# Optimization experiments

Measured on AMD Instinct MI355X. Metric: run time of the kernel, lower is better.

## Reference

```python
import jax, jax.numpy as jnp
import numpy as np

B, IN_DIM, EMBED_DIM = 8192, 2048, 256
H1, H2 = 1024, 512
CODEBOOK_SIZE, N_LAYERS = 1024, 3
TEMP, COMMIT_W = 1.25, 0.25


def _l2norm(x, eps=1e-12):
    # F.normalize: x / max(||x||, eps)
    n = jnp.linalg.norm(x, axis=-1, keepdims=True)
    return x / jnp.maximum(n, eps)


def _layernorm(x, g, b, eps=1e-5):
    mu = x.mean(-1, keepdims=True)
    var = x.var(-1, keepdims=True)  # biased, matches torch LayerNorm
    return (x - mu) / jnp.sqrt(var + eps) * g + b


def _mlp(x, w1, g1, b1, w2, g2, b2, w3, normalize):
    h = _layernorm(jax.nn.silu(x @ w1), g1, b1)
    h = _layernorm(jax.nn.silu(h @ w2), g2, b2)
    h = h @ w3
    return _l2norm(h) if normalize else h


def _quantize(res, codebook, key):
    # squared euclidean distances [B, K], scaled by temperature
    dist = ((res ** 2).sum(1, keepdims=True)
            + (codebook ** 2).sum(1)[None, :]
            - 2.0 * res @ codebook.T) / TEMP
    # torch.multinomial(softmax(-dist)) == categorical with logits -dist
    ids = jax.random.categorical(key, -dist, axis=1)
    emb = codebook[ids]  # [B, D] gather
    sg = jax.lax.stop_gradient
    u = res / (jnp.linalg.norm(res, axis=-1, keepdims=True) + 1e-8)
    q = emb / (jnp.linalg.norm(emb, axis=-1, keepdims=True) + 1e-8)
    w = sg(_l2norm(u + q, eps=1e-6))
    # rotation trick: e - 2(e.w)w + 2(e.u)q  (w, u, q detached)
    emb_out = (res
               - 2.0 * (res * w).sum(-1, keepdims=True) * w
               + 2.0 * (res * sg(u)).sum(-1, keepdims=True) * sg(q))
    # QuantizeLoss (sum-reduced MSE both directions)
    loss = ((sg(res) - emb) ** 2).sum() + COMMIT_W * ((res - sg(emb)) ** 2).sum()
    return emb_out, ids, loss


def setup_inputs() -> dict:
    key = jax.random.key(0)
    ks = jax.random.split(key, 8)
    def lin(k, fan_in, fan_out):
        return (jax.random.normal(k, (fan_in, fan_out), jnp.float32)
                / np.sqrt(fan_in).astype(np.float32))
    return {
        "x": jax.random.normal(ks[0], (B, IN_DIM), jnp.float32),
        "enc_w1": lin(ks[1], IN_DIM, H1),
        "enc_g1": jnp.ones((H1,), jnp.float32),
        "enc_b1": jnp.zeros((H1,), jnp.float32),
        "enc_w2": lin(ks[2], H1, H2),
        "enc_g2": jnp.ones((H2,), jnp.float32),
        "enc_b2": jnp.zeros((H2,), jnp.float32),
        "enc_w3": lin(ks[3], H2, EMBED_DIM),
        "dec_w1": lin(ks[4], EMBED_DIM, H2),
        "dec_g1": jnp.ones((H2,), jnp.float32),
        "dec_b1": jnp.zeros((H2,), jnp.float32),
        "dec_w2": lin(ks[5], H2, H1),
        "dec_g2": jnp.ones((H1,), jnp.float32),
        "dec_b2": jnp.zeros((H1,), jnp.float32),
        "dec_w3": lin(ks[6], H1, IN_DIM),
        # nn.init.uniform_ -> U[0,1)
        "codebooks": jax.random.uniform(ks[7], (N_LAYERS, CODEBOOK_SIZE, EMBED_DIM), jnp.float32),
    }


def reference(x, enc_w1, enc_g1, enc_b1, enc_w2, enc_g2, enc_b2, enc_w3,
              dec_w1, dec_g1, dec_b1, dec_w2, dec_g2, dec_b2, dec_w3,
              codebooks):
    res = _mlp(x, enc_w1, enc_g1, enc_b1, enc_w2, enc_g2, enc_b2, enc_w3,
               normalize=False)
    keys = jax.random.split(jax.random.key(42), N_LAYERS)
    quant_loss = jnp.float32(0.0)
    embs, sem = [], []
    for i in range(N_LAYERS):  # small fixed residual depth
        e, ids, l = _quantize(res, codebooks[i], keys[i])
        quant_loss = quant_loss + l
        res = res - e
        embs.append(e)
        sem.append(ids)
    embs_arr = jnp.stack(embs, axis=-1)   # [B, D, L]
    sem_ids = jnp.stack(sem, axis=-1)     # [B, L]
    x_hat = _mlp(embs_arr.sum(-1), dec_w1, dec_g1, dec_b1, dec_w2, dec_g2,
                 dec_b2, dec_w3, normalize=True)
    recon = ((x_hat - x) ** 2).sum(-1)    # per-sample [B]
    loss = (recon + quant_loss).mean()
    embs_norm = jnp.linalg.norm(embs_arr, axis=1)  # [B, L]
    eq = (sem_ids[:, None, :] == sem_ids[None, :, :]).all(-1)  # [B, B]
    p_unique = (~jnp.triu(eq, k=1)).all(1).sum() / sem_ids.shape[0]
    return loss, recon.mean(), quant_loss, embs_norm, p_unique
```

## Files before the change

kernel.cpp:

```cpp
#include <hip/hip_runtime.h>
#include <hip/hip_bf16.h>
#include <stdint.h>
#include <math.h>

#define NB    8192
#define INDIM 2048
#define EMB   256
#define H1N   1024
#define H2N   512
#define KCB   1024
#define NLAYER 3
#define HASHN 16384

typedef _Float16 f16x8 __attribute__((ext_vector_type(8)));
typedef _Float16 f16x4 __attribute__((ext_vector_type(4)));
typedef _Float16 f16x2 __attribute__((ext_vector_type(2)));
typedef float    f32x4 __attribute__((ext_vector_type(4)));

#define LO_SCALE 1024.0f
#define LO_INV   (1.0f / 1024.0f)

#define GLD16(g, p) __builtin_amdgcn_global_load_lds( \
    (const __attribute__((address_space(1))) void*)(g), \
    (__attribute__((address_space(3))) void*)(p), 16, 0, 0)

__host__ __device__ inline void tf2x32(uint32_t k0, uint32_t k1, uint32_t x0, uint32_t x1,
                                       uint32_t& o0, uint32_t& o1)
{
  const uint32_t ks2 = 0x1BD11BDAu ^ k0 ^ k1;
  uint32_t a = x0 + k0, b = x1 + k1;
#define TF_RND(r) { a += b; b = (b << (r)) | (b >> (32 - (r))); b ^= a; }
  TF_RND(13) TF_RND(15) TF_RND(26) TF_RND(6)
  a += k1; b += ks2 + 1u;
  TF_RND(17) TF_RND(29) TF_RND(16) TF_RND(24)
  a += ks2; b += k0 + 2u;
  TF_RND(13) TF_RND(15) TF_RND(26) TF_RND(6)
  a += k0; b += k1 + 3u;
  TF_RND(17) TF_RND(29) TF_RND(16) TF_RND(24)
  a += k1; b += ks2 + 4u;
  TF_RND(13) TF_RND(15) TF_RND(26) TF_RND(6)
  a += ks2; b += k0 + 5u;
#undef TF_RND
  o0 = a; o1 = b;
}

__device__ inline float blk_reduce_sum(float v, float* sbuf)
{
  const int t = threadIdx.x;
  sbuf[t] = v; __syncthreads();
  for (int s = 128; s > 0; s >>= 1) {
    if (t < s) sbuf[t] += sbuf[t + s];
    __syncthreads();
  }
  float r = sbuf[0];
  __syncthreads();
  return r;
}

template<int NS, int OUTMODE, int BM>
__global__ __launch_bounds__(BM == 256 ? 512 : 256) void mgemm(
    const _Float16* __restrict__ A0, const _Float16* __restrict__ A1,
    const _Float16* __restrict__ B0, const _Float16* __restrict__ B1,
    void* __restrict__ Cp, _Float16* __restrict__ Cs0, _Float16* __restrict__ Cs1,
    float* __restrict__ pval, int* __restrict__ pidx, const float* __restrict__ cn2l,
    uint32_t gk0, uint32_t gk1,
    int M, int N, int K)
{
  constexpr int WAVES = (BM == 256) ? 8 : 4;
  constexpr int RPR = WAVES * 16;
  constexpr int AR = BM / RPR;
  constexpr int BR = 128 / RPR;
  constexpr int JN = (BM == 64) ? 2 : 4;
  constexpr int ASPL = BM * 64;
  constexpr int ABYTES = NS * ASPL;
  constexpr int BBYTES = NS * 8192;
  constexpr int BUF = ABYTES + BBYTES;
  __shared__ __align__(16) char sm[2 * BUF];

  const int nwg = gridDim.x * gridDim.y;
  const int bid0 = blockIdx.y * gridDim.x + blockIdx.x;
  const int cpx = nwg >> 3;
  const int swz = (bid0 & 7) * cpx + (bid0 >> 3);
  const int bx = swz % gridDim.x, by = swz / gridDim.x;

  const int tid = threadIdx.x;
  const int w = tid >> 6, l = tid & 63;
  const int wm = (BM == 64) ? 0 : (w >> 1);
  const int wn = (BM == 64) ? w : (w & 1);
  constexpr int WCOL = (BM == 64) ? 32 : 64;
  const size_t brow = (size_t)by * BM;
  const size_t bcol = (size_t)bx * 128;

  const int brow16 = w * 16 + (l >> 2);
  const int bcol16 = ((l & 3) ^ ((l >> 3) & 3)) * 8;

  const _Float16* gA0 = A0 + (brow + brow16) * (size_t)K + bcol16;
  const _Float16* gA1 = (NS >= 2) ? (A1 + (brow + brow16) * (size_t)K + bcol16) : nullptr;
  const _Float16* gB0 = B0 + (bcol + brow16) * (size_t)K + bcol16;
  const _Float16* gB1 = (NS >= 2) ? (B1 + (bcol + brow16) * (size_t)K + bcol16) : nullptr;

  auto STAGE = [&](int buf, int kk) {
    char* bA = sm + buf * BUF;
    char* bB = bA + ABYTES;
#pragma unroll
    for (int i = 0; i < AR; i++) {
      GLD16(gA0 + (size_t)(i * RPR) * K + kk, bA + i * (RPR * 64) + w * 1024);
      if constexpr (NS >= 2) GLD16(gA1 + (size_t)(i * RPR) * K + kk, bA + ASPL + i * (RPR * 64) + w * 1024);
    }
#pragma unroll
    for (int i = 0; i < BR; i++) {
      GLD16(gB0 + (size_t)(i * RPR) * K + kk, bB + i * (RPR * 64) + w * 1024);
      if constexpr (NS >= 2) GLD16(gB1 + (size_t)(i * RPR) * K + kk, bB + 8192 + i * (RPR * 64) + w * 1024);
    }
  };

  f32x4 acc0[4][JN], acc1[4][JN];
#pragma unroll
  for (int i = 0; i < 4; i++)
#pragma unroll
    for (int j = 0; j < JN; j++) {
      acc0[i][j] = (f32x4){0.f, 0.f, 0.f, 0.f};
      if constexpr (NS >= 2) acc1[i][j] = (f32x4){0.f, 0.f, 0.f, 0.f};
    }

  const int srow = l & 15;
  const int ksel = l >> 4;
  const int sel2 = (srow >> 1) & 3;
  const int fslot16 = (ksel ^ sel2) * 16;

  STAGE(0, 0);
  __syncthreads();
  int cur = 0;

  for (int k0 = 0; k0 < K; k0 += 32) {
    if (k0 + 32 < K) STAGE(cur ^ 1, k0 + 32);

    const char* smA = sm + cur * BUF;
    const char* smB = smA + ABYTES;

    f16x8 ah[4], al[4];
#pragma unroll
    for (int i = 0; i < 4; i++) {
      const int rb = (wm * 64 + i * 16 + srow) * 64 + fslot16;
      ah[i] = *(const f16x8*)(smA + rb);
      if constexpr (NS >= 2) al[i] = *(const f16x8*)(smA + ASPL + rb);
    }

#pragma unroll
    for (int j = 0; j < JN; j++) {
      const int rb = (wn * WCOL + j * 16 + srow) * 64 + fslot16;
      f16x8 bh = *(const f16x8*)(smB + rb);
      f16x8 bl{};
      if constexpr (NS >= 2) bl = *(const f16x8*)(smB + 8192 + rb);
#pragma unroll
      for (int i = 0; i < 4; i++) {
        acc0[i][j] = __builtin_amdgcn_mfma_f32_16x16x32_f16(ah[i], bh, acc0[i][j], 0, 0, 0);
        if constexpr (NS >= 2) {
          acc1[i][j] = __builtin_amdgcn_mfma_f32_16x16x32_f16(ah[i], bl, acc1[i][j], 0, 0, 0);
          acc1[i][j] = __builtin_amdgcn_mfma_f32_16x16x32_f16(al[i], bh, acc1[i][j], 0, 0, 0);
        }
      }
    }
    __syncthreads();
    cur ^= 1;
  }

  if constexpr (OUTMODE == 3) {
    const int rowb = (int)brow + wm * 64 + (l >> 4) * 4;
    const int colb = (int)bcol + wn * 64 + (l & 15);
#pragma unroll
    for (int i = 0; i < 4; i++)
#pragma unroll
      for (int r = 0; r < 4; r++) {
        const int grow = rowb + i * 16 + r;
        float bestv = -INFINITY; int bestj = 0x7fffffff;
#pragma unroll
        for (int j = 0; j < JN; j++) {
          float v = acc0[i][j][r];
          if constexpr (NS >= 2) v += acc1[i][j][r] * LO_INV;
          const int gcol = colb + j * 16;
          const uint32_t idx = (uint32_t)(grow * KCB + gcol);
          uint32_t o0, o1;
          tf2x32(gk0, gk1, 0u, idx, o0, o1);
          const uint32_t bits = o0 ^ o1;
          float f = __uint_as_float((bits >> 9) | 0x3f800000u) - 1.0f;
          float u = fmaxf(f, 1.17549435e-38f);
          float gmb = -__logf(-__logf(u));
          float val = gmb + (2.0f * v - cn2l[gcol]) / 1.25f;
          if (val > bestv || (val == bestv && gcol < bestj)) { bestv = val; bestj = gcol; }
        }
#pragma unroll
        for (int m = 1; m < 16; m <<= 1) {
          float ov = __shfl_xor(bestv, m);
          int oj = __shfl_xor(bestj, m);
          if (ov > bestv || (ov == bestv && oj < bestj)) { bestv = ov; bestj = oj; }
        }
        if ((l & 15) == 0) {
          const int slot = bx * 2 + wn;
          pval[(size_t)grow * 16 + slot] = bestv;
          pidx[(size_t)grow * 16 + slot] = bestj;
        }
      }
  } else {
    const int crow0 = wm * 64 + (l >> 4) * 4;
    const int ccol0 = wn * WCOL + (l & 15);
#pragma unroll
    for (int i = 0; i < 4; i++)
#pragma unroll
      for (int j = 0; j < JN; j++)
#pragma unroll
        for (int r = 0; r < 4; r++) {
          float v = acc0[i][j][r];
          if constexpr (NS >= 2) v += acc1[i][j][r] * LO_INV;
          const size_t row = brow + crow0 + i * 16 + r;
          const size_t col = bcol + ccol0 + j * 16;
          const size_t o = row * N + col;
          if constexpr (OUTMODE == 0) {
            ((float*)Cp)[o] = v;
          } else if constexpr (OUTMODE == 1) {
            ((_Float16*)Cp)[o] = (_Float16)v;
          } else {
            ((float*)Cp)[o] = v;
            _Float16 h = (_Float16)v;
            Cs0[o] = h;
            Cs1[o] = (_Float16)((v - (float)h) * LO_SCALE);
          }
        }
  }
}

struct PrepArgs {
  const float* w[6];
  _Float16* t0[6];
  _Float16* t1[6];
  int K[6], N[6];
  int off[7];
  const float* x;
  _Float16* xh; _Float16* xl;
  const float* cb;
  _Float16* cbh; _Float16* cbl;
  float* cn2;
  int cvtBlocks;
};

__global__ __launch_bounds__(256) void prep_all(PrepArgs P)
{
  __shared__ float shf[33 * 32];
  const int b = blockIdx.x, t = threadIdx.x;

  if (b < P.off[6]) {
    int j = 0;
    while (b >= P.off[j + 1]) j++;
    const int lb = b - P.off[j];
    const int K = P.K[j], N = P.N[j];
    const int nbx = N / 32;
    const int nb = (lb % nbx) * 32, kb = (lb / nbx) * 32;
    const float* Wsrc = P.w[j];
    _Float16* T0 = P.t0[j];
    _Float16* T1 = P.t1[j];
    const int tx = t & 31, ty = t >> 5;
#pragma unroll
    for (int i = 0; i < 32; i += 8)
      shf[(ty + i) * 33 + tx] = Wsrc[(size_t)(kb + ty + i) * N + nb + tx];
    __syncthreads();
#pragma unroll
    for (int i = 0; i < 32; i += 8) {
      float v = shf[tx * 33 + ty + i];
      size_t o = (size_t)(nb + ty + i) * K + kb + tx;
      _Float16 h = (_Float16)v;
      T0[o] = h;
      if (T1) T1[o] = (_Float16)((v - (float)h) * LO_SCALE);
    }
  } else if (b < P.off[6] + P.cvtBlocks) {
    const int i = ((b - P.off[6]) * 256 + t) * 8;
    float4 va = *(const float4*)(P.x + i);
    float4 vb = *(const float4*)(P.x + i + 4);
    float f[8] = {va.x, va.y, va.z, va.w, vb.x, vb.y, vb.z, vb.w};
    f16x8 hv, lv;
#pragma unroll
    for (int e = 0; e < 8; e++) {
      _Float16 h = (_Float16)f[e];
      hv[e] = h;
      lv[e] = (_Float16)((f[e] - (float)h) * LO_SCALE);
    }
    *(f16x8*)(P.xh + i) = hv;
    *(f16x8*)(P.xl + i) = lv;
  } else {
    const int r = b - P.off[6] - P.cvtBlocks;
    const size_t o = (size_t)r * EMB + t;
    const float v = P.cb[o];
    _Float16 h = (_Float16)v;
    P.cbh[o] = h;
    P.cbl[o] = (_Float16)((v - (float)h) * LO_SCALE);
    float s = blk_reduce_sum(v * v, shf);
    if (t == 0) P.cn2[r] = s;
  }
}

template<int NCOL, int NS>
__global__ __launch_bounds__(256) void silu_ln(const float* __restrict__ in,
                                               const float* __restrict__ g,
                                               const float* __restrict__ bta,
                                               _Float16* __restrict__ o0,
                                               _Float16* __restrict__ o1)
{
  constexpr int PT = NCOL / 256;
  __shared__ float sb[256];
  const int b = blockIdx.x, t = threadIdx.x;
  const float* row = in + (size_t)b * NCOL;
  const int c0 = t * PT;
  float v[PT];
  if constexpr (PT == 4) {
    float4 xv = *(const float4*)(row + c0);
    v[0] = xv.x; v[1] = xv.y; v[2] = xv.z; v[3] = xv.w;
  } else {
    float2 xv = *(const float2*)(row + c0);
    v[0] = xv.x; v[1] = xv.y;
  }
  float s = 0.f;
#pragma unroll
  for (int i = 0; i < PT; i++) {
    float sv = v[i] / (1.f + expf(-v[i]));
    v[i] = sv; s += sv;
  }
  s = blk_reduce_sum(s, sb);
  const float mu = s / (float)NCOL;
  float q = 0.f;
#pragma unroll
  for (int i = 0; i < PT; i++) { float d = v[i] - mu; q += d * d; }
  q = blk_reduce_sum(q, sb);
  const float inv = 1.f / sqrtf(q / (float)NCOL + 1e-5f);

  float gv[PT], bv[PT];
  if constexpr (PT == 4) {
    float4 g4 = *(const float4*)(g + c0);
    float4 b4 = *(const float4*)(bta + c0);
    gv[0]=g4.x; gv[1]=g4.y; gv[2]=g4.z; gv[3]=g4.w;
    bv[0]=b4.x; bv[1]=b4.y; bv[2]=b4.z; bv[3]=b4.w;
  } else {
    float2 g2 = *(const float2*)(g + c0);
    float2 b2 = *(const float2*)(bta + c0);
    gv[0]=g2.x; gv[1]=g2.y; bv[0]=b2.x; bv[1]=b2.y;
  }
  const size_t ob = (size_t)b * NCOL + c0;
  if constexpr (PT == 4) {
    f16x4 h4, l4;
#pragma unroll
    for (int i = 0; i < 4; i++) {
      float y = (v[i] - mu) * inv * gv[i] + bv[i];
      _Float16 h = (_Float16)y;
      h4[i] = h;
      if constexpr (NS >= 2) l4[i] = (_Float16)((y - (float)h) * LO_SCALE);
    }
    *(f16x4*)(o0 + ob) = h4;
    if constexpr (NS >= 2) *(f16x4*)(o1 + ob) = l4;
  } else {
    f16x2 h2, l2;
#pragma unroll
    for (int i = 0; i < 2; i++) {
      float y = (v[i] - mu) * inv * gv[i] + bv[i];
      _Float16 h = (_Float16)y;
      h2[i] = h;
      if constexpr (NS >= 2) l2[i] = (_Float16)((y - (float)h) * LO_SCALE);
    }
    *(f16x2*)(o0 + ob) = h2;
    if constexpr (NS >= 2) *(f16x2*)(o1 + ob) = l2;
  }
}

__global__ __launch_bounds__(256) void sample_update(
    const float* __restrict__ pval, const int* __restrict__ pidx,
    const float* __restrict__ cbf,
    float* __restrict__ res, float* __restrict__ esum,
    float* __restrict__ qrow, float* __restrict__ outEn,
    _Float16* __restrict__ r0, _Float16* __restrict__ r1,
    _Float16* __restrict__ esumb, int* __restrict__ ids,
    uint32_t* __restrict__ packed, int layer)
{
  __shared__ float sv[256];
  __shared__ int   si[256];
  const int b = blockIdx.x, t = threadIdx.x;

  float best = -INFINITY; int bestj = 0x7fffffff;
  if (t < 16) { best = pval[(size_t)b * 16 + t]; bestj = pidx[(size_t)b * 16 + t]; }
  sv[t] = best; si[t] = bestj; __syncthreads();
  for (int s = 128; s > 0; s >>= 1) {
    if (t < s) {
      float v2 = sv[t + s]; int j2 = si[t + s];
      if (v2 > sv[t] || (v2 == sv[t] && j2 < si[t])) { sv[t] = v2; si[t] = j2; }
    }
    __syncthreads();
  }
  const int id = si[0];
  if (t == 0) {
    ids[b * NLAYER + layer] = id;
    if (layer == NLAYER - 1)
      packed[b] = (uint32_t)ids[b * NLAYER] | ((uint32_t)ids[b * NLAYER + 1] << 10)
                | ((uint32_t)id << 20);
  }
  __syncthreads();

  const size_t idx = (size_t)b * EMB + t;
  const float r = res[idx];
  const float e_ = cbf[(size_t)id * EMB + t];

  const float rn2 = blk_reduce_sum(r * r, sv);
  const float en2 = blk_reduce_sum(e_ * e_, sv);
  const float rn = sqrtf(rn2), en = sqrtf(en2);
  const float u = r / (rn + 1e-8f);
  const float q = e_ / (en + 1e-8f);
  const float sm = u + q;
  const float sn2 = blk_reduce_sum(sm * sm, sv);
  const float w = sm / fmaxf(sqrtf(sn2), 1e-6f);
  const float rw = blk_reduce_sum(r * w, sv);
  const float ru = blk_reduce_sum(r * u, sv);
  const float e = r - 2.f * rw * w + 2.f * ru * q;
  const float eo2 = blk_reduce_sum(e * e, sv);
  const float dq = r - e_;
  const float ql = blk_reduce_sum(dq * dq, sv);

  if (t == 0) {
    outEn[b * NLAYER + layer] = sqrtf(eo2);
    if (layer == 0) qrow[b] = 1.25f * ql; else qrow[b] += 1.25f * ql;
  }
  const float nr = r - e;
  res[idx] = nr;
  if (layer != NLAYER - 1) {
    _Float16 h = (_Float16)nr;
    r0[idx] = h;
    r1[idx] = (_Float16)((nr - (float)h) * LO_SCALE);
  }
  float ns = (layer == 0) ? e : esum[idx] + e;
  esum[idx] = ns;
  if (layer == NLAYER - 1) esumb[idx] = (_Float16)ns;
}

__global__ __launch_bounds__(256) void l2norm_recon(const _Float16* __restrict__ y,
                                                    const float* __restrict__ x,
                                                    float* __restrict__ recon)
{
  __shared__ float sb[256];
  const int b = blockIdx.x, t = threadIdx.x;
  const _Float16* yr = y + (size_t)b * INDIM;
  const float* xr = x + (size_t)b * INDIM;
  f16x8 v = *(const f16x8*)&yr[t * 8];
  float vy[8];
  float ss = 0.f;
#pragma unroll
  for (int i = 0; i < 8; i++) { vy[i] = (float)v[i]; ss += vy[i] * vy[i]; }
  ss = blk_reduce_sum(ss, sb);
  const float inv = 1.f / fmaxf(sqrtf(ss), 1e-12f);
  float4 xa = *(const float4*)&xr[t * 8];
  float4 xb = *(const float4*)&xr[t * 8 + 4];
  float xf[8] = {xa.x, xa.y, xa.z, xa.w, xb.x, xb.y, xb.z, xb.w};
  float acc = 0.f;
#pragma unroll
  for (int i = 0; i < 8; i++) {
    float d = vy[i] * inv - xf[i];
    acc += d * d;
  }
  acc = blk_reduce_sum(acc, sb);
  if (t == 0) recon[b] = acc;
}

__global__ __launch_bounds__(256) void finalize2(const float* __restrict__ recon,
                                                 const float* __restrict__ qrow,
                                                 const uint32_t* __restrict__ packed,
                                                 float* __restrict__ out)
{
  __shared__ uint32_t tab[HASHN];
  __shared__ double sd[256];
  __shared__ int    si[256];
  const int t = threadIdx.x;
  for (int i = t; i < HASHN; i += 256) tab[i] = 0xFFFFFFFFu;
  __syncthreads();

  int my = 0;
  double aR = 0.0, aQ = 0.0;
  for (int i = t; i < NB; i += 256) {
    aR += (double)recon[i];
    aQ += (double)qrow[i];
    const uint32_t v = packed[i];
    uint32_t h = (v * 2654435761u) & (HASHN - 1);
    while (true) {
      uint32_t old = atomicCAS(&tab[h], 0xFFFFFFFFu, v);
      if (old == 0xFFFFFFFFu) { my++; break; }
      if (old == v) break;
      h = (h + 1) & (HASHN - 1);
    }
  }
  sd[t] = aR; si[t] = my; __syncthreads();
  for (int s = 128; s > 0; s >>= 1) {
    if (t < s) { sd[t] += sd[t + s]; si[t] += si[t + s]; }
    __syncthreads();
  }
  const double sumR = sd[0]; const int dcnt = si[0]; __syncthreads();
  sd[t] = aQ; __syncthreads();
  for (int s = 128; s > 0; s >>= 1) { if (t < s) sd[t] += sd[t + s]; __syncthreads(); }
  const double sumQ = sd[0];
  if (t == 0) {
    const float rm = (float)(sumR / (double)NB);
    const float ql = (float)sumQ;
    out[0] = rm + ql;
    out[1] = rm;
    out[2] = ql;
    out[3 + NB * NLAYER] = (float)dcnt / (float)NB;
  }
}

extern "C" void kernel_launch(void* const* d_in, const int* in_sizes, int n_in,
                              void* d_out, int out_size, void* d_ws, size_t ws_size,
                              hipStream_t stream)
{
  const float* x      = (const float*)d_in[0];
  const float* enc_w1 = (const float*)d_in[1];
  const float* enc_g1 = (const float*)d_in[2];
  const float* enc_b1 = (const float*)d_in[3];
  const float* enc_w2 = (const float*)d_in[4];
  const float* enc_g2 = (const float*)d_in[5];
  const float* enc_b2 = (const float*)d_in[6];
  const float* enc_w3 = (const float*)d_in[7];
  const float* dec_w1 = (const float*)d_in[8];
  const float* dec_g1 = (const float*)d_in[9];
  const float* dec_b1 = (const float*)d_in[10];
  const float* dec_w2 = (const float*)d_in[11];
  const float* dec_g2 = (const float*)d_in[12];
  const float* dec_b2 = (const float*)d_in[13];
  const float* dec_w3 = (const float*)d_in[14];
  const float* codebooks = (const float*)d_in[15];
  float* out = (float*)d_out;

  char* W = (char*)d_ws;
  _Float16* xh   = (_Float16*)(W + 0);
  _Float16* h1n0 = (_Float16*)(W + 0);
  _Float16* h1n1 = (_Float16*)(W + 16777216);
  _Float16* h2n0 = (_Float16*)(W + 0);
  _Float16* h2n1 = (_Float16*)(W + 8388608);
  _Float16* res0 = (_Float16*)(W + 16777216);
  _Float16* res1 = (_Float16*)(W + 20971520);
  _Float16* d1n  = (_Float16*)(W + 0);
  _Float16* d2n  = (_Float16*)(W + 25165824);
  _Float16* xl    = (_Float16*)(W + 33554432);
  float*    h2    = (float*)  (W + 33554432);
  float*    d1    = (float*)  (W + 33554432);
  float*    res32 = (float*)  (W + 50331648);
  float*    esum32= (float*)  (W + 58720256);
  float*    h1 = (float*)    (W + 67108864);
  float*    d2 = (float*)    (W + 67108864);
  _Float16* yb = (_Float16*) (W + 67108864);
  _Float16* w1t0 = (_Float16*)(W + 100663296);
  _Float16* w1t1 = (_Float16*)(W + 104857600);
  _Float16* w2t0 = (_Float16*)(W + 109051904);
  _Float16* w2t1 = (_Float16*)(W + 110100480);
  _Float16* w3t0 = (_Float16*)(W + 111149056);
  _Float16* w3t1 = (_Float16*)(W + 111411200);
  _Float16* dw1t = (_Float16*)(W + 111673344);
  _Float16* dw2t = (_Float16*)(W + 111935488);
  _Float16* dw3t = (_Float16*)(W + 112984064);
  _Float16* cbh  = (_Float16*)(W + 117178368);
  _Float16* cbl  = (_Float16*)(W + 118751232);
  _Float16* esumb= (_Float16*)(W + 120324096);
  float* cn2   = (float*)(W + 124518400);
  float* recon = (float*)(W + 124534784);
  float* qrow  = (float*)(W + 124567552);
  int*   ids   = (int*)  (W + 124600320);
  uint32_t* packed = (uint32_t*)(W + 124698624);
  float*    pval   = (float*)   (W + 124850176);
  int*      pidx   = (int*)     (W + 125374464);

  uint32_t key0[NLAYER], key1[NLAYER];
  for (int l = 0; l < NLAYER; l++) tf2x32(0u, 42u, 0u, (uint32_t)l, key0[l], key1[l]);

  dim3 blk(256), blk512(512);
  PrepArgs P;
  P.w[0] = enc_w1; P.t0[0] = w1t0; P.t1[0] = w1t1; P.K[0] = INDIM; P.N[0] = H1N;
  P.w[1] = enc_w2; P.t0[1] = w2t0; P.t1[1] = w2t1; P.K[1] = H1N;   P.N[1] = H2N;
  P.w[2] = enc_w3; P.t0[2] = w3t0; P.t1[2] = w3t1; P.K[2] = H2N;   P.N[2] = EMB;
  P.w[3] = dec_w1; P.t0[3] = dw1t; P.t1[3] = nullptr; P.K[3] = EMB; P.N[3] = H2N;
  P.w[4] = dec_w2; P.t0[4] = dw2t; P.t1[4] = nullptr; P.K[4] = H2N; P.N[4] = H1N;
  P.w[5] = dec_w3; P.t0[5] = dw3t; P.t1[5] = nullptr; P.K[5] = H1N; P.N[5] = INDIM;
  P.off[0] = 0;
  for (int j = 0; j < 6; j++) P.off[j + 1] = P.off[j] + (P.N[j] / 32) * (P.K[j] / 32);
  P.x = x; P.xh = xh; P.xl = xl;
  P.cb = codebooks; P.cbh = cbh; P.cbl = cbl; P.cn2 = cn2;
  P.cvtBlocks = (NB * INDIM) / 2048;
  const int prepGrid = P.off[6] + P.cvtBlocks + NLAYER * KCB;
  prep_all<<<prepGrid, blk, 0, stream>>>(P);

  mgemm<2,0,256><<<dim3(H1N/128, NB/256), blk512, 0, stream>>>(xh, xl, w1t0, w1t1,
      h1, nullptr, nullptr, nullptr, nullptr, nullptr, 0u, 0u, NB, H1N, INDIM);
  silu_ln<H1N,2><<<NB, blk, 0, stream>>>(h1, enc_g1, enc_b1, h1n0, h1n1);
  mgemm<2,0,128><<<dim3(H2N/128, NB/128), blk, 0, stream>>>(h1n0, h1n1, w2t0, w2t1,
      h2, nullptr, nullptr, nullptr, nullptr, nullptr, 0u, 0u, NB, H2N, H1N);
  silu_ln<H2N,2><<<NB, blk, 0, stream>>>(h2, enc_g2, enc_b2, h2n0, h2n1);
  mgemm<2,2,64><<<dim3(EMB/128, NB/64), blk, 0, stream>>>(h2n0, h2n1, w3t0, w3t1,
      res32, res0, res1, nullptr, nullptr, nullptr, 0u, 0u, NB, EMB, H2N);

  for (int l = 0; l < NLAYER; l++) {
    const float* cbfl = codebooks + (size_t)l * KCB * EMB;
    const size_t co = (size_t)l * KCB * EMB;
    mgemm<2,3,256><<<dim3(KCB/128, NB/256), blk512, 0, stream>>>(res0, res1,
        cbh + co, cbl + co, nullptr, nullptr, nullptr,
        pval, pidx, cn2 + l * KCB, key0[l], key1[l], NB, KCB, EMB);
    sample_update<<<NB, blk, 0, stream>>>(pval, pidx, cbfl,
        res32, esum32, qrow, out + 3, res0, res1, esumb, ids, packed, l);
  }

  mgemm<1,0,128><<<dim3(H2N/128, NB/128), blk, 0, stream>>>(esumb, nullptr, dw1t, nullptr,
      d1, nullptr, nullptr, nullptr, nullptr, nullptr, 0u, 0u, NB, H2N, EMB);
  silu_ln<H2N,1><<<NB, blk, 0, stream>>>(d1, dec_g1, dec_b1, d1n, nullptr);
  mgemm<1,0,128><<<dim3(H1N/128, NB/128), blk, 0, stream>>>(d1n, nullptr, dw2t, nullptr,
      d2, nullptr, nullptr, nullptr, nullptr, nullptr, 0u, 0u, NB, H1N, H2N);
  silu_ln<H1N,1><<<NB, blk, 0, stream>>>(d2, dec_g2, dec_b2, d2n, nullptr);
  mgemm<1,1,256><<<dim3(INDIM/128, NB/256), blk512, 0, stream>>>(d2n, nullptr, dw3t, nullptr,
      yb, nullptr, nullptr, nullptr, nullptr, nullptr, 0u, 0u, NB, INDIM, H1N);
  l2norm_recon<<<NB, blk, 0, stream>>>(yb, x, recon);

  finalize2<<<1, blk, 0, stream>>>(recon, qrow, packed, out);
}
```

Baseline: 615.7 us.

## Use packed atomicMax argmax, wave-per-row reductions, and fp16 decoder intermediates

```diff
diff --git a/kernel.cpp b/kernel.cpp
--- a/kernel.cpp
+++ b/kernel.cpp
@@ -57,12 +57,19 @@
   return r;
 }
 
+__device__ inline float wred(float v)
+{
+#pragma unroll
+  for (int m = 32; m > 0; m >>= 1) v += __shfl_xor(v, m);
+  return v;
+}
+
 template<int NS, int OUTMODE, int BM>
 __global__ __launch_bounds__(BM == 256 ? 512 : 256) void mgemm(
     const _Float16* __restrict__ A0, const _Float16* __restrict__ A1,
     const _Float16* __restrict__ B0, const _Float16* __restrict__ B1,
     void* __restrict__ Cp, _Float16* __restrict__ Cs0, _Float16* __restrict__ Cs1,
-    float* __restrict__ pval, int* __restrict__ pidx, const float* __restrict__ cn2l,
+    unsigned long long* __restrict__ amax, const float* __restrict__ cn2l,
     uint32_t gk0, uint32_t gk1,
     int M, int N, int K)
 {
@@ -196,9 +203,11 @@
           if (ov > bestv || (ov == bestv && oj < bestj)) { bestv = ov; bestj = oj; }
         }
         if ((l & 15) == 0) {
-          const int slot = bx * 2 + wn;
-          pval[(size_t)grow * 16 + slot] = bestv;
-          pidx[(size_t)grow * 16 + slot] = bestj;
+          uint32_t mb = __float_as_uint(bestv);
+          mb = (mb & 0x80000000u) ? ~mb : (mb | 0x80000000u);
+          unsigned long long pk = ((unsigned long long)mb << 32)
+                                | (unsigned long long)(uint32_t)(~(uint32_t)bestj);
+          atomicMax(amax + grow, pk);
         }
       }
   } else {
@@ -240,6 +249,7 @@
   const float* cb;
   _Float16* cbh; _Float16* cbl;
   float* cn2;
+  unsigned long long* amax;
   int cvtBlocks;
 };
 
@@ -285,7 +295,7 @@
     }
     *(f16x8*)(P.xh + i) = hv;
     *(f16x8*)(P.xl + i) = lv;
-  } else {
+  } else if (b < P.off[6] + P.cvtBlocks + NLAYER * KCB) {
     const int r = b - P.off[6] - P.cvtBlocks;
     const size_t o = (size_t)r * EMB + t;
     const float v = P.cb[o];
@@ -294,11 +304,14 @@
     P.cbl[o] = (_Float16)((v - (float)h) * LO_SCALE);
     float s = blk_reduce_sum(v * v, shf);
     if (t == 0) P.cn2[r] = s;
-  }
-}
-
-template<int NCOL, int NS>
-__global__ __launch_bounds__(256) void silu_ln(const float* __restrict__ in,
+  } else {
+    const int i = (b - P.off[6] - P.cvtBlocks - NLAYER * KCB) * 256 + t;
+    if (i < NB) P.amax[i] = 0ull;
+  }
+}
+
+template<int NCOL, int NS, int IN16>
+__global__ __launch_bounds__(256) void silu_ln(const void* __restrict__ inp,
                                                const float* __restrict__ g,
                                                const float* __restrict__ bta,
                                                _Float16* __restrict__ o0,
@@ -307,15 +320,27 @@
   constexpr int PT = NCOL / 256;
   __shared__ float sb[256];
   const int b = blockIdx.x, t = threadIdx.x;
-  const float* row = in + (size_t)b * NCOL;
   const int c0 = t * PT;
   float v[PT];
-  if constexpr (PT == 4) {
-    float4 xv = *(const float4*)(row + c0);
-    v[0] = xv.x; v[1] = xv.y; v[2] = xv.z; v[3] = xv.w;
+  if constexpr (IN16) {
+    const _Float16* row = (const _Float16*)inp + (size_t)b * NCOL;
+    if constexpr (PT == 4) {
+      f16x4 xv = *(const f16x4*)(row + c0);
+#pragma unroll
+      for (int i = 0; i < 4; i++) v[i] = (float)xv[i];
+    } else {
+      f16x2 xv = *(const f16x2*)(row + c0);
+      v[0] = (float)xv[0]; v[1] = (float)xv[1];
+    }
   } else {
-    float2 xv = *(const float2*)(row + c0);
-    v[0] = xv.x; v[1] = xv.y;
+    const float* row = (const float*)inp + (size_t)b * NCOL;
+    if constexpr (PT == 4) {
+      float4 xv = *(const float4*)(row + c0);
+      v[0] = xv.x; v[1] = xv.y; v[2] = xv.z; v[3] = xv.w;
+    } else {
+      float2 xv = *(const float2*)(row + c0);
+      v[0] = xv.x; v[1] = xv.y;
+    }
   }
   float s = 0.f;
 #pragma unroll
@@ -369,7 +394,7 @@
 }
 
 __global__ __launch_bounds__(256) void sample_update(
-    const float* __restrict__ pval, const int* __restrict__ pidx,
+    unsigned long long* __restrict__ amax,
     const float* __restrict__ cbf,
     float* __restrict__ res, float* __restrict__ esum,
     float* __restrict__ qrow, float* __restrict__ outEn,
@@ -377,90 +402,125 @@
     _Float16* __restrict__ esumb, int* __restrict__ ids,
     uint32_t* __restrict__ packed, int layer)
 {
-  __shared__ float sv[256];
-  __shared__ int   si[256];
-  const int b = blockIdx.x, t = threadIdx.x;
-
-  float best = -INFINITY; int bestj = 0x7fffffff;
-  if (t < 16) { best = pval[(size_t)b * 16 + t]; bestj = pidx[(size_t)b * 16 + t]; }
-  sv[t] = best; si[t] = bestj; __syncthreads();
-  for (int s = 128; s > 0; s >>= 1) {
-    if (t < s) {
-      float v2 = sv[t + s]; int j2 = si[t + s];
-      if (v2 > sv[t] || (v2 == sv[t] && j2 < si[t])) { sv[t] = v2; si[t] = j2; }
-    }
-    __syncthreads();
-  }
-  const int id = si[0];
-  if (t == 0) {
+  const int t = threadIdx.x, w = t >> 6, l = t & 63;
+  const int b = blockIdx.x * 4 + w;
+
+  const unsigned long long pk = amax[b];
+  const int id = (int)(~(uint32_t)(pk & 0xFFFFFFFFull));
+  if (l == 0) {
     ids[b * NLAYER + layer] = id;
     if (layer == NLAYER - 1)
       packed[b] = (uint32_t)ids[b * NLAYER] | ((uint32_t)ids[b * NLAYER + 1] << 10)
                 | ((uint32_t)id << 20);
-  }
-  __syncthreads();
-
-  const size_t idx = (size_t)b * EMB + t;
-  const float r = res[idx];
-  const float e_ = cbf[(size_t)id * EMB + t];
-
-  const float rn2 = blk_reduce_sum(r * r, sv);
-  const float en2 = blk_reduce_sum(e_ * e_, sv);
+    else
+      amax[b] = 0ull;
+  }
+
+  const size_t base = (size_t)b * EMB + l * 4;
+  float4 r4 = *(const float4*)(res + base);
+  float4 e4 = *(const float4*)(cbf + (size_t)id * EMB + l * 4);
+  float r_[4] = {r4.x, r4.y, r4.z, r4.w};
+  float e_[4] = {e4.x, e4.y, e4.z, e4.w};
+
+  float a0 = 0.f, a1 = 0.f;
+#pragma unroll
+  for (int i = 0; i < 4; i++) { a0 += r_[i] * r_[i]; a1 += e_[i] * e_[i]; }
+  const float rn2 = wred(a0), en2 = wred(a1);
   const float rn = sqrtf(rn2), en = sqrtf(en2);
-  const float u = r / (rn + 1e-8f);
-  const float q = e_ / (en + 1e-8f);
-  const float sm = u + q;
-  const float sn2 = blk_reduce_sum(sm * sm, sv);
-  const float w = sm / fmaxf(sqrtf(sn2), 1e-6f);
-  const float rw = blk_reduce_sum(r * w, sv);
-  const float ru = blk_reduce_sum(r * u, sv);
-  const float e = r - 2.f * rw * w + 2.f * ru * q;
-  const float eo2 = blk_reduce_sum(e * e, sv);
-  const float dq = r - e_;
-  const float ql = blk_reduce_sum(dq * dq, sv);
-
-  if (t == 0) {
+  float u_[4], q_[4], s_[4];
+  float a2 = 0.f;
+#pragma unroll
+  for (int i = 0; i < 4; i++) {
+    u_[i] = r_[i] / (rn + 1e-8f);
+    q_[i] = e_[i] / (en + 1e-8f);
+    s_[i] = u_[i] + q_[i];
+    a2 += s_[i] * s_[i];
+  }
+  const float sn2 = wred(a2);
+  const float wn_ = 1.f / fmaxf(sqrtf(sn2), 1e-6f);
+  float a3 = 0.f, a4 = 0.f;
+#pragma unroll
+  for (int i = 0; i < 4; i++) {
+    a3 += r_[i] * s_[i] * wn_;
+    a4 += r_[i] * u_[i];
+  }
+  const float rw = wred(a3), ru = wred(a4);
+  float eo[4];
+  float a5 = 0.f, a6 = 0.f;
+#pragma unroll
+  for (int i = 0; i < 4; i++) {
+    eo[i] = r_[i] - 2.f * rw * (s_[i] * wn_) + 2.f * ru * q_[i];
+    a5 += eo[i] * eo[i];
+    float dq = r_[i] - e_[i];
+    a6 += dq * dq;
+  }
+  const float eo2 = wred(a5), ql = wred(a6);
+
+  if (l == 0) {
     outEn[b * NLAYER + layer] = sqrtf(eo2);
     if (layer == 0) qrow[b] = 1.25f * ql; else qrow[b] += 1.25f * ql;
   }
-  const float nr = r - e;
-  res[idx] = nr;
+
+  float nr[4];
+#pragma unroll
+  for (int i = 0; i < 4; i++) nr[i] = r_[i] - eo[i];
   if (layer != NLAYER - 1) {
-    _Float16 h = (_Float16)nr;
-    r0[idx] = h;
-    r1[idx] = (_Float16)((nr - (float)h) * LO_SCALE);
-  }
-  float ns = (layer == 0) ? e : esum[idx] + e;
-  esum[idx] = ns;
-  if (layer == NLAYER - 1) esumb[idx] = (_Float16)ns;
+    *(float4*)(res + base) = make_float4(nr[0], nr[1], nr[2], nr[3]);
+    f16x4 h4, l4;
+#pragma unroll
+    for (int i = 0; i < 4; i++) {
+      _Float16 h = (_Float16)nr[i];
+      h4[i] = h;
+      l4[i] = (_Float16)((nr[i] - (float)h) * LO_SCALE);
+    }
+    *(f16x4*)(r0 + base) = h4;
+    *(f16x4*)(r1 + base) = l4;
+  }
+  float ns[4];
+#pragma unroll
+  for (int i = 0; i < 4; i++) ns[i] = (layer == 0) ? eo[i] : esum[base + i] + eo[i];
+  if (layer != NLAYER - 1) {
+    *(float4*)(esum + base) = make_float4(ns[0], ns[1], ns[2], ns[3]);
+  } else {
+    f16x4 h4;
+#pragma unroll
+    for (int i = 0; i < 4; i++) h4[i] = (_Float16)ns[i];
+    *(f16x4*)(esumb + base) = h4;
+  }
 }
 
 __global__ __launch_bounds__(256) void l2norm_recon(const _Float16* __restrict__ y,
                                                     const float* __restrict__ x,
                                                     float* __restrict__ recon)
 {
-  __shared__ float sb[256];
-  const int b = blockIdx.x, t = threadIdx.x;
+  const int t = threadIdx.x, w = t >> 6, l = t & 63;
+  const int b = blockIdx.x * 4 + w;
   const _Float16* yr = y + (size_t)b * INDIM;
   const float* xr = x + (size_t)b * INDIM;
-  f16x8 v = *(const f16x8*)&yr[t * 8];
-  float vy[8];
+
+  float vy[32], xf[32];
   float ss = 0.f;
 #pragma unroll
-  for (int i = 0; i < 8; i++) { vy[i] = (float)v[i]; ss += vy[i] * vy[i]; }
-  ss = blk_reduce_sum(ss, sb);
+  for (int i = 0; i < 4; i++) {
+    const int c = l * 8 + i * 512;
+    f16x8 v8 = *(const f16x8*)(yr + c);
+    float4 xa = *(const float4*)(xr + c);
+    float4 xb = *(const float4*)(xr + c + 4);
+    xf[i*8+0]=xa.x; xf[i*8+1]=xa.y; xf[i*8+2]=xa.z; xf[i*8+3]=xa.w;
+    xf[i*8+4]=xb.x; xf[i*8+5]=xb.y; xf[i*8+6]=xb.z; xf[i*8+7]=xb.w;
+#pragma unroll
+    for (int j = 0; j < 8; j++) { vy[i*8+j] = (float)v8[j]; ss += vy[i*8+j] * vy[i*8+j]; }
+  }
+  ss = wred(ss);
   const float inv = 1.f / fmaxf(sqrtf(ss), 1e-12f);
-  float4 xa = *(const float4*)&xr[t * 8];
-  float4 xb = *(const float4*)&xr[t * 8 + 4];
-  float xf[8] = {xa.x, xa.y, xa.z, xa.w, xb.x, xb.y, xb.z, xb.w};
   float acc = 0.f;
 #pragma unroll
-  for (int i = 0; i < 8; i++) {
+  for (int i = 0; i < 32; i++) {
     float d = vy[i] * inv - xf[i];
     acc += d * d;
   }
-  acc = blk_reduce_sum(acc, sb);
-  if (t == 0) recon[b] = acc;
+  acc = wred(acc);
+  if (l == 0) recon[b] = acc;
 }
 
 __global__ __launch_bounds__(256) void finalize2(const float* __restrict__ recon,
@@ -542,11 +602,11 @@
   _Float16* d2n  = (_Float16*)(W + 25165824);
   _Float16* xl    = (_Float16*)(W + 33554432);
   float*    h2    = (float*)  (W + 33554432);
-  float*    d1    = (float*)  (W + 33554432);
+  _Float16* d1h   = (_Float16*)(W + 33554432);
   float*    res32 = (float*)  (W + 50331648);
   float*    esum32= (float*)  (W + 58720256);
   float*    h1 = (float*)    (W + 67108864);
-  float*    d2 = (float*)    (W + 67108864);
+  _Float16* d2h = (_Float16*)(W + 67108864);
   _Float16* yb = (_Float16*) (W + 67108864);
   _Float16* w1t0 = (_Float16*)(W + 100663296);
   _Float16* w1t1 = (_Float16*)(W + 104857600);
@@ -565,8 +625,7 @@
   float* qrow  = (float*)(W + 124567552);
   int*   ids   = (int*)  (W + 124600320);
   uint32_t* packed = (uint32_t*)(W + 124698624);
-  float*    pval   = (float*)   (W + 124850176);
-  int*      pidx   = (int*)     (W + 125374464);
+  unsigned long long* amax = (unsigned long long*)(W + 124850176);
 
   uint32_t key0[NLAYER], key1[NLAYER];
   for (int l = 0; l < NLAYER; l++) tf2x32(0u, 42u, 0u, (uint32_t)l, key0[l], key1[l]);
@@ -583,38 +642,39 @@
   for (int j = 0; j < 6; j++) P.off[j + 1] = P.off[j] + (P.N[j] / 32) * (P.K[j] / 32);
   P.x = x; P.xh = xh; P.xl = xl;
   P.cb = codebooks; P.cbh = cbh; P.cbl = cbl; P.cn2 = cn2;
+  P.amax = amax;
   P.cvtBlocks = (NB * INDIM) / 2048;
-  const int prepGrid = P.off[6] + P.cvtBlocks + NLAYER * KCB;
+  const int prepGrid = P.off[6] + P.cvtBlocks + NLAYER * KCB + NB / 256;
   prep_all<<<prepGrid, blk, 0, stream>>>(P);
 
   mgemm<2,0,256><<<dim3(H1N/128, NB/256), blk512, 0, stream>>>(xh, xl, w1t0, w1t1,
-      h1, nullptr, nullptr, nullptr, nullptr, nullptr, 0u, 0u, NB, H1N, INDIM);
-  silu_ln<H1N,2><<<NB, blk, 0, stream>>>(h1, enc_g1, enc_b1, h1n0, h1n1);
+      h1, nullptr, nullptr, nullptr, nullptr, 0u, 0u, NB, H1N, INDIM);
+  silu_ln<H1N,2,0><<<NB, blk, 0, stream>>>(h1, enc_g1, enc_b1, h1n0, h1n1);
   mgemm<2,0,128><<<dim3(H2N/128, NB/128), blk, 0, stream>>>(h1n0, h1n1, w2t0, w2t1,
-      h2, nullptr, nullptr, nullptr, nullptr, nullptr, 0u, 0u, NB, H2N, H1N);
-  silu_ln<H2N,2><<<NB, blk, 0, stream>>>(h2, enc_g2, enc_b2, h2n0, h2n1);
+      h2, nullptr, nullptr, nullptr, nullptr, 0u, 0u, NB, H2N, H1N);
+  silu_ln<H2N,2,0><<<NB, blk, 0, stream>>>(h2, enc_g2, enc_b2, h2n0, h2n1);
   mgemm<2,2,64><<<dim3(EMB/128, NB/64), blk, 0, stream>>>(h2n0, h2n1, w3t0, w3t1,
-      res32, res0, res1, nullptr, nullptr, nullptr, 0u, 0u, NB, EMB, H2N);
+      res32, res0, res1, nullptr, nullptr, 0u, 0u, NB, EMB, H2N);
 
   for (int l = 0; l < NLAYER; l++) {
     const float* cbfl = codebooks + (size_t)l * KCB * EMB;
     const size_t co = (size_t)l * KCB * EMB;
     mgemm<2,3,256><<<dim3(KCB/128, NB/256), blk512, 0, stream>>>(res0, res1,
         cbh + co, cbl + co, nullptr, nullptr, nullptr,
-        pval, pidx, cn2 + l * KCB, key0[l], key1[l], NB, KCB, EMB);
-    sample_update<<<NB, blk, 0, stream>>>(pval, pidx, cbfl,
+        amax, cn2 + l * KCB, key0[l], key1[l], NB, KCB, EMB);
+    sample_update<<<NB/4, blk, 0, stream>>>(amax, cbfl,
         res32, esum32, qrow, out + 3, res0, res1, esumb, ids, packed, l);
   }
 
-  mgemm<1,0,128><<<dim3(H2N/128, NB/128), blk, 0, stream>>>(esumb, nullptr, dw1t, nullptr,
-      d1, nullptr, nullptr, nullptr, nullptr, nullptr, 0u, 0u, NB, H2N, EMB);
-  silu_ln<H2N,1><<<NB, blk, 0, stream>>>(d1, dec_g1, dec_b1, d1n, nullptr);
-  mgemm<1,0,128><<<dim3(H1N/128, NB/128), blk, 0, stream>>>(d1n, nullptr, dw2t, nullptr,
-      d2, nullptr, nullptr, nullptr, nullptr, nullptr, 0u, 0u, NB, H1N, H2N);
-  silu_ln<H1N,1><<<NB, blk, 0, stream>>>(d2, dec_g2, dec_b2, d2n, nullptr);
+  mgemm<1,1,128><<<dim3(H2N/128, NB/128), blk, 0, stream>>>(esumb, nullptr, dw1t, nullptr,
+      d1h, nullptr, nullptr, nullptr, nullptr, 0u, 0u, NB, H2N, EMB);
+  silu_ln<H2N,1,1><<<NB, blk, 0, stream>>>(d1h, dec_g1, dec_b1, d1n, nullptr);
+  mgemm<1,1,128><<<dim3(H1N/128, NB/128), blk, 0, stream>>>(d1n, nullptr, dw2t, nullptr,
+      d2h, nullptr, nullptr, nullptr, nullptr, 0u, 0u, NB, H1N, H2N);
+  silu_ln<H1N,1,1><<<NB, blk, 0, stream>>>(d2h, dec_g2, dec_b2, d2n, nullptr);
   mgemm<1,1,256><<<dim3(INDIM/128, NB/256), blk512, 0, stream>>>(d2n, nullptr, dw3t, nullptr,
-      yb, nullptr, nullptr, nullptr, nullptr, nullptr, 0u, 0u, NB, INDIM, H1N);
-  l2norm_recon<<<NB, blk, 0, stream>>>(yb, x, recon);
+      yb, nullptr, nullptr, nullptr, nullptr, 0u, 0u, NB, INDIM, H1N);
+  l2norm_recon<<<NB/4, blk, 0, stream>>>(yb, x, recon);
 
   finalize2<<<1, blk, 0, stream>>>(recon, qrow, packed, out);
 }
```

Measured after the change: 549.2 us. -10.8%, faster.
